# Optimization experiments

Measured on AMD Instinct MI355X. Metric: run time of the kernel, lower is better.

Reference implementation:

```python
import jax, jax.numpy as jnp
import numpy as np

EPS = 1e-6
LN_EPS = 1e-5   # torch nn.LayerNorm default eps
BN_EPS = 1e-5   # torch nn.BatchNorm1d default eps
NUM_HEADS = 8
NEG_SLOPE = 0.0  # leaky=0 in TransformerBlock


def vn_linear(x, W, b, eps=1e-6):
    # x: [B, Cin, 3, N], W: [Cin, Cout], b: [Cout, 3]
    out = jnp.einsum('bidn,io->bodn', x, W)
    u = eps * b / jnp.linalg.norm(b, axis=1, keepdims=True)  # [Cout,3]
    return out + u[None, :, :, None]


def vn_layer_norm(x, gamma, beta):
    # x: [B, C, 3, N]; LayerNorm over channel dim of the vector norms
    norm = jnp.linalg.norm(x, axis=2) + EPS            # [B, C, N]
    t = jnp.swapaxes(norm, 1, 2)                       # [B, N, C]
    mu = t.mean(axis=-1, keepdims=True)
    var = ((t - mu) ** 2).mean(axis=-1, keepdims=True)
    ln = (t - mu) / jnp.sqrt(var + LN_EPS) * gamma + beta
    norm_ln = jnp.swapaxes(ln, 1, 2)                   # [B, C, N]
    return x / norm[:, :, None, :] * norm_ln[:, :, None, :]


def vn_batch_norm(x, gamma, beta):
    # training-mode BatchNorm1d over channel dim of the vector norms
    norm = jnp.linalg.norm(x, axis=2) + EPS            # [B, C, N]
    mu = norm.mean(axis=(0, 2), keepdims=True)         # [1, C, 1]
    var = ((norm - mu) ** 2).mean(axis=(0, 2), keepdims=True)
    bn = (norm - mu) / jnp.sqrt(var + BN_EPS) * gamma[None, :, None] + beta[None, :, None]
    return x / norm[:, :, None, :] * bn[:, :, None, :]


def vn_leaky_relu(x, W, negative_slope=NEG_SLOPE):
    d = jnp.einsum('bidn,io->bodn', x, W)              # learned direction
    dot = (x * d).sum(axis=2, keepdims=True)           # [B, C, 1, N]
    d_norm_sq = (d * d).sum(axis=2, keepdims=True)
    proj = x - dot / (d_norm_sq + EPS) * d
    pos = jnp.where(dot >= 0, x, proj)
    return negative_slope * x + (1.0 - negative_slope) * pos


def attention(Q, K, Z, Wq, bq, Wk, bk, Wz, bz, Wo, bo, num_heads=NUM_HEADS):
    B, C, _, M = Q.shape
    N = K.shape[-1]
    Ch = C // num_heads
    q = vn_linear(Q, Wq, bq).reshape(B, num_heads, Ch, 3, M)
    k = vn_linear(K, Wk, bk).reshape(B, num_heads, Ch, 3, N)
    z = vn_linear(Z, Wz, bz).reshape(B, num_heads, Ch, 3, N)
    # Frobenius inner product: merge (Ch,3) -> F
    qf = q.reshape(B, num_heads, Ch * 3, M)
    kf = k.reshape(B, num_heads, Ch * 3, N)
    const = 1.0 / np.sqrt(3 * Ch)
    scores = const * jnp.einsum('bhfm,bhfn->bhmn', qf, kf)
    A = jax.nn.softmax(scores, axis=-1)
    out = jnp.einsum('bhcdn,bhmn->bhcdm', z, A).reshape(B, C, 3, M)
    return vn_linear(out, Wo, bo)


def forward(x, Wq, bq, Wk, bk, Wz, bz, Wo, bo, ln1_g, ln1_b,
            Wm1, bm1, bn_g, bn_b, Wr, Wm2, bm2, ln2_g, ln2_b):
    queries = x
    y = attention(queries, x, x, Wq, bq, Wk, bk, Wz, bz, Wo, bo)
    y = vn_layer_norm(y, ln1_g, ln1_b)
    y = y + queries
    identity = y
    h = vn_linear(y, Wm1, bm1)
    h = vn_batch_norm(h, bn_g, bn_b)
    h = vn_leaky_relu(h, Wr)
    h = vn_linear(h, Wm2, bm2)
    h = vn_layer_norm(h, ln2_g, ln2_b)
    return h + identity


def setup_inputs() -> dict:
    key = jax.random.key(0)
    ks = list(jax.random.split(key, 16))
    B, C, N = 8, 256, 1024
    bound = 1.0 / np.sqrt(C)

    def lin(k, fin, fout):
        k1, k2 = jax.random.split(k)
        W = jax.random.uniform(k1, (fin, fout), minval=-bound, maxval=bound, dtype=jnp.float32)
        b = jax.random.uniform(k2, (fout, 3), minval=-bound, maxval=bound, dtype=jnp.float32)
        return W, b

    x = jax.random.normal(ks[0], (B, C, 3, N), dtype=jnp.float32)
    Wq, bq = lin(ks[1], C, C)
    Wk, bk = lin(ks[2], C, C)
    Wz, bz = lin(ks[3], C, C)
    Wo, bo = lin(ks[4], C, C)
    Wm1, bm1 = lin(ks[5], C, C)
    Wm2, bm2 = lin(ks[6], C, C)
    Wr = jax.random.uniform(ks[7], (C, C), minval=-bound, maxval=bound, dtype=jnp.float32)
    ones = jnp.ones((C,), jnp.float32)
    zeros = jnp.zeros((C,), jnp.float32)
    return dict(x=x, Wq=Wq, bq=bq, Wk=Wk, bk=bk, Wz=Wz, bz=bz, Wo=Wo, bo=bo,
                ln1_g=ones, ln1_b=zeros, Wm1=Wm1, bm1=bm1, bn_g=ones, bn_b=zeros,
                Wr=Wr, Wm2=Wm2, bm2=bm2, ln2_g=ones, ln2_b=zeros)


def reference(x, Wq, bq, Wk, bk, Wz, bz, Wo, bo, ln1_g, ln1_b,
              Wm1, bm1, bn_g, bn_b, Wr, Wm2, bm2, ln2_g, ln2_b):
    return forward(x, Wq, bq, Wk, bk, Wz, bz, Wo, bo, ln1_g, ln1_b,
                   Wm1, bm1, bn_g, bn_b, Wr, Wm2, bm2, ln2_g, ln2_b)
```

## Files before the change

kernel.cpp:

```cpp
#include <hip/hip_runtime.h>
#include <math.h>

typedef __attribute__((ext_vector_type(8))) short bf16x8;
typedef __attribute__((ext_vector_type(4))) float f32x4;
typedef unsigned short u16;
typedef __attribute__((ext_vector_type(4))) unsigned short u16x4;
typedef __attribute__((ext_vector_type(8))) unsigned short u16x8;

#define VN_EPS 1e-6f
#define LN_EPS 1e-5f
#define BN_EPS 1e-5f
#define ISQ 0.10206207261596575f

__device__ __forceinline__ u16 f2bf(float f) {
    unsigned u = __builtin_bit_cast(unsigned, f);
    return (u16)((u + 0x7FFFu + ((u >> 16) & 1u)) >> 16);
}
__device__ __forceinline__ float bf2f(u16 h) {
    unsigned u = ((unsigned)h) << 16;
    return __builtin_bit_cast(float, u);
}

__global__ __launch_bounds__(256) void k_u(
    const float* __restrict__ b0, const float* __restrict__ b1,
    const float* __restrict__ b2, const float* __restrict__ b3,
    const float* __restrict__ b4, const float* __restrict__ b5,
    float* __restrict__ uall)
{
    const float* bs[6] = {b0, b1, b2, b3, b4, b5};
    const float* bp = bs[blockIdx.x];
    const int co = threadIdx.x;
    const float v0 = bp[co*3+0], v1 = bp[co*3+1], v2 = bp[co*3+2];
    const float inv = rsqrtf(v0*v0 + v1*v1 + v2*v2);
    float* u = uall + blockIdx.x*768 + co*3;
    u[0] = VN_EPS*v0*inv; u[1] = VN_EPS*v1*inv; u[2] = VN_EPS*v2*inv;
}

__global__ __launch_bounds__(256) void k_wtrans(
    const float* __restrict__ w0, const float* __restrict__ w1,
    const float* __restrict__ w2, const float* __restrict__ w3,
    const float* __restrict__ w4, const float* __restrict__ w5,
    const float* __restrict__ w6, u16* __restrict__ wth, u16* __restrict__ wtl)
{
    const int wi = blockIdx.z;
    const float* W = (wi==0)?w0:(wi==1)?w1:(wi==2)?w2:(wi==3)?w3:(wi==4)?w4:(wi==5)?w5:w6;
    u16* WtH = wth + (long)wi*65536;
    u16* WtL = wtl + (long)wi*65536;
    const int i0 = blockIdx.y*64, o0 = blockIdx.x*64;
    __shared__ float st[64][67];
    const int t = threadIdx.x, q = t >> 6, lane = t & 63;
    for (int j = 0; j < 16; ++j) {
        const int i = q*16 + j;
        st[i][lane] = W[(i0 + i)*256 + o0 + lane];
    }
    __syncthreads();
    for (int j = 0; j < 16; ++j) {
        const int o = q*16 + j;
        const float v = st[lane][o];
        const u16 hi = f2bf(v);
        WtH[(o0 + o)*256 + i0 + lane] = hi;
        WtL[(o0 + o)*256 + i0 + lane] = f2bf(v - bf2f(hi));
    }
}

template<int MODE>
__global__ __launch_bounds__(256) void k_cgemm(
    const float* __restrict__ X, const u16* __restrict__ WtH, const u16* __restrict__ WtL,
    const float* __restrict__ U,
    float* __restrict__ OutF, u16* __restrict__ OutH, u16* __restrict__ OutL)
{
    __shared__ u16 sh[32768];
    const int tid = threadIdx.x;
    const int b = blockIdx.z / 3, d = blockIdx.z % 3;
    const int n0 = blockIdx.x * 64;
    const int co0 = blockIdx.y * 64;

    {
        const int tn = (tid & 15) * 4;
        const int ti = (tid >> 4) * 4;
        #pragma unroll
        for (int it = 0; it < 4; ++it) {
            const int i_l = it*64 + ti;
            const long rb = (((long)(b*256 + i_l))*3 + d)*1024 + n0 + tn;
            const float4 r0 = *(const float4*)&X[rb];
            const float4 r1 = *(const float4*)&X[rb + 3072];
            const float4 r2 = *(const float4*)&X[rb + 6144];
            const float4 r3 = *(const float4*)&X[rb + 9216];
            const float vals[4][4] = {
                {r0.x, r1.x, r2.x, r3.x},
                {r0.y, r1.y, r2.y, r3.y},
                {r0.z, r1.z, r2.z, r3.z},
                {r0.w, r1.w, r2.w, r3.w}};
            #pragma unroll
            for (int j = 0; j < 4; ++j) {
                const int n = tn + j;
                u16x4 hv, lv;
                #pragma unroll
                for (int e = 0; e < 4; ++e) {
                    const float v = vals[j][e];
                    const u16 hi = f2bf(v);
                    hv[e] = hi;
                    lv[e] = f2bf(v - bf2f(hi));
                }
                const int slot = i_l >> 3;
                const int idx = n*256 + ((((slot ^ (n & 7)) << 3)) | (i_l & 4));
                *(u16x4*)&sh[idx] = hv;
                *(u16x4*)&sh[16384 + idx] = lv;
            }
        }
    }
    __syncthreads();

    const int w = tid >> 6, l = tid & 63;
    const int lr = l & 15, lg = l >> 4;

    f32x4 zero = {0.f, 0.f, 0.f, 0.f};
    f32x4 acc[4] = {zero, zero, zero, zero};

    const long arow = (long)(co0 + w*16 + lr)*256 + lg*8;
    #pragma unroll
    for (int s = 0; s < 8; ++s) {
        const bf16x8 ah = *(const bf16x8*)(WtH + arow + s*32);
        const bf16x8 al = *(const bf16x8*)(WtL + arow + s*32);
        #pragma unroll
        for (int ni = 0; ni < 4; ++ni) {
            const int row = ni*16 + lr;
            const int slot = s*4 + lg;
            const int idx = row*256 + ((slot ^ (row & 7)) << 3);
            const bf16x8 bh_ = *(const bf16x8*)&sh[idx];
            const bf16x8 bl_ = *(const bf16x8*)&sh[16384 + idx];
            acc[ni] = __builtin_amdgcn_mfma_f32_16x16x32_bf16(ah, bh_, acc[ni], 0, 0, 0);
            acc[ni] = __builtin_amdgcn_mfma_f32_16x16x32_bf16(ah, bl_, acc[ni], 0, 0, 0);
            acc[ni] = __builtin_amdgcn_mfma_f32_16x16x32_bf16(al, bh_, acc[ni], 0, 0, 0);
        }
    }

    if constexpr (MODE == 0) {
        #pragma unroll
        for (int ni = 0; ni < 4; ++ni)
            #pragma unroll
            for (int r = 0; r < 4; ++r) {
                const int co = co0 + w*16 + lg*4 + r;
                const int nn = n0 + ni*16 + lr;
                float v = acc[ni][r];
                if (U) v += U[co*3 + d];
                OutF[(((long)(b*256 + co))*3 + d)*1024 + nn] = v;
            }
    } else if constexpr (MODE == 1) {
        #pragma unroll
        for (int ni = 0; ni < 4; ++ni)
            #pragma unroll
            for (int r = 0; r < 4; ++r) {
                const int co = co0 + w*16 + lg*4 + r;
                const int nn = n0 + ni*16 + lr;
                float v = acc[ni][r] + U[co*3 + d];
                const long idx = (((long)(b*256 + co))*3 + d)*1024 + nn;
                const u16 hi = f2bf(v);
                OutH[idx] = hi;
                OutL[idx] = f2bf(v - bf2f(hi));
            }
    } else {
        __syncthreads();
        u16* olh = sh;
        u16* oll = sh + 8448;
        #pragma unroll
        for (int ni = 0; ni < 4; ++ni)
            #pragma unroll
            for (int r = 0; r < 4; ++r) {
                const int co_l = w*16 + lg*4 + r;
                float v = acc[ni][r] + U[(co0 + co_l)*3 + d];
                const u16 hi = f2bf(v);
                olh[co_l*66 + ni*16 + lr] = hi;
                oll[co_l*66 + ni*16 + lr] = f2bf(v - bf2f(hi));
            }
        __syncthreads();
        const int n_l = tid & 63, grp = tid >> 6;
        const int h = (co0 >> 5) + (grp >> 1);
        const long base = ((long)(b*8 + h)*1024 + n0 + n_l)*96 + d*32 + (grp & 1)*16;
        u16x8 v0h, v1h, v0l, v1l;
        #pragma unroll
        for (int p = 0; p < 8; ++p) {
            v0h[p] = olh[(grp*16 + p)*66 + n_l];
            v1h[p] = olh[(grp*16 + 8 + p)*66 + n_l];
            v0l[p] = oll[(grp*16 + p)*66 + n_l];
            v1l[p] = oll[(grp*16 + 8 + p)*66 + n_l];
        }
        *(u16x8*)&OutH[base]     = v0h;
        *(u16x8*)&OutH[base + 8] = v1h;
        *(u16x8*)&OutL[base]     = v0l;
        *(u16x8*)&OutL[base + 8] = v1l;
    }
}

__global__ __launch_bounds__(256) void k_attn(
    const u16* __restrict__ Qh, const u16* __restrict__ Ql,
    const u16* __restrict__ Kh, const u16* __restrict__ Kl,
    const u16* __restrict__ Zh, const u16* __restrict__ Zl,
    float* __restrict__ Ao)
{
    const int i = blockIdx.x;
    const int xcd = i & 7;
    const int j = i >> 3;
    const int bh = xcd*8 + (j >> 6);
    const int mt = j & 63;
    const int b = bh >> 3, h = bh & 7;
    const int m0 = mt*16;
    const int tid = threadIdx.x;
    const int w = tid >> 6, l = tid & 63, lr = l & 15, lg = l >> 4;

    __shared__ float S[16*1024];
    __shared__ float outl[16*100];
    __shared__ float inv16[16];

    f32x4 zero = {0.f, 0.f, 0.f, 0.f};

    const long qbase = ((long)bh*1024 + m0 + lr)*96 + lg*8;
    bf16x8 qhf[3], qlf[3];
    #pragma unroll
    for (int s = 0; s < 3; ++s) {
        qhf[s] = *(const bf16x8*)(Qh + qbase + s*32);
        qlf[s] = *(const bf16x8*)(Ql + qbase + s*32);
    }
    for (int nf = 0; nf < 16; ++nf) {
        const int n0 = w*256 + nf*16;
        const long kb = ((long)bh*1024 + n0 + lr)*96 + lg*8;
        f32x4 acc = zero;
        #pragma unroll
        for (int s = 0; s < 3; ++s) {
            const bf16x8 khf = *(const bf16x8*)(Kh + kb + s*32);
            const bf16x8 klf = *(const bf16x8*)(Kl + kb + s*32);
            acc = __builtin_amdgcn_mfma_f32_16x16x32_bf16(qhf[s], khf, acc, 0, 0, 0);
            acc = __builtin_amdgcn_mfma_f32_16x16x32_bf16(qhf[s], klf, acc, 0, 0, 0);
            acc = __builtin_amdgcn_mfma_f32_16x16x32_bf16(qlf[s], khf, acc, 0, 0, 0);
        }
        #pragma unroll
        for (int r = 0; r < 4; ++r)
            S[(lg*4 + r)*1024 + n0 + lr] = acc[r] * ISQ;
    }
    __syncthreads();

    {
        const int r = tid >> 4, s = tid & 15;
        float preg[64];
        float mx = -1e30f;
        #pragma unroll
        for (int j2 = 0; j2 < 64; ++j2) {
            preg[j2] = S[r*1024 + j2*16 + s];
            mx = fmaxf(mx, preg[j2]);
        }
        #pragma unroll
        for (int off = 1; off < 16; off <<= 1)
            mx = fmaxf(mx, __shfl_xor(mx, off));
        float sm = 0.f;
        #pragma unroll
        for (int j2 = 0; j2 < 64; ++j2) {
            const float p = __expf(preg[j2] - mx);
            preg[j2] = p;
            sm += p;
        }
        #pragma unroll
        for (int off = 1; off < 16; off <<= 1)
            sm += __shfl_xor(sm, off);
        if (s == 0) inv16[r] = 1.0f / sm;
        __syncthreads();
        char* Sb = (char*)S;
        #pragma unroll
        for (int j2 = 0; j2 < 64; ++j2) {
            const int n = j2*16 + s;
            const u16 hi = f2bf(preg[j2]);
            const u16 lo = f2bf(preg[j2] - bf2f(hi));
            const int byoff = (n*2) ^ ((r & 7) << 4);
            *(u16*)(Sb + r*4096 + byoff)        = hi;
            *(u16*)(Sb + r*4096 + 2048 + byoff) = lo;
        }
    }
    __syncthreads();

    f32x4 acc2[6];
    #pragma unroll
    for (int f = 0; f < 6; ++f) acc2[f] = zero;
    const long zrow = (long)(b*768 + h*96);
    const char* Sb = (const char*)S;
    for (int kb = 0; kb < 8; ++kb) {
        const int n = w*256 + kb*32 + lg*8;
        const int byoff = lr*4096 + (((n*2)) ^ ((lr & 7) << 4));
        const bf16x8 ph = *(const bf16x8*)(Sb + byoff);
        const bf16x8 pl = *(const bf16x8*)(Sb + byoff + 2048);
        #pragma unroll
        for (int ff = 0; ff < 6; ++ff) {
            const long zb = (zrow + ff*16 + lr)*1024 + n;
            const bf16x8 azh = *(const bf16x8*)(Zh + zb);
            const bf16x8 azl = *(const bf16x8*)(Zl + zb);
            acc2[ff] = __builtin_amdgcn_mfma_f32_16x16x32_bf16(ph, azh, acc2[ff], 0, 0, 0);
            acc2[ff] = __builtin_amdgcn_mfma_f32_16x16x32_bf16(ph, azl, acc2[ff], 0, 0, 0);
            acc2[ff] = __builtin_amdgcn_mfma_f32_16x16x32_bf16(pl, azh, acc2[ff], 0, 0, 0);
        }
    }
    __syncthreads();
    for (int wv = 0; wv < 4; ++wv) {
        if (w == wv) {
            #pragma unroll
            for (int ff = 0; ff < 6; ++ff)
                #pragma unroll
                for (int r = 0; r < 4; ++r) {
                    const int m = lg*4 + r, f = ff*16 + lr;
                    if (wv == 0) outl[m*100 + f] = acc2[ff][r];
                    else         outl[m*100 + f] += acc2[ff][r];
                }
        }
        __syncthreads();
    }
    for (int idx = tid; idx < 384; idx += 256) {
        const int f = idx >> 2, mg = idx & 3;
        float4 o;
        o.x = outl[(mg*4+0)*100 + f] * inv16[mg*4+0];
        o.y = outl[(mg*4+1)*100 + f] * inv16[mg*4+1];
        o.z = outl[(mg*4+2)*100 + f] * inv16[mg*4+2];
        o.w = outl[(mg*4+3)*100 + f] * inv16[mg*4+3];
        *(float4*)&Ao[(long)(b*768 + h*96 + f)*1024 + m0 + mg*4] = o;
    }
}

__global__ __launch_bounds__(256) void k_vnln(
    const float* __restrict__ X, const float* __restrict__ Res,
    const float* __restrict__ g, const float* __restrict__ be,
    float* __restrict__ Out)
{
    const int b  = blockIdx.x >> 5;
    const int n  = ((blockIdx.x & 31) << 5) + threadIdx.x;
    const int ty = threadIdx.y;
    const long bbase = (long)b * (256*3*1024);
    float sum = 0.0f, sq = 0.0f;
    for (int ci = 0; ci < 32; ++ci) {
        const int c = (ty << 5) + ci;
        const long base = bbase + (long)c*3072 + n;
        const float x0 = X[base], x1 = X[base+1024], x2 = X[base+2048];
        const float nr = sqrtf(x0*x0 + x1*x1 + x2*x2) + VN_EPS;
        sum += nr; sq += nr*nr;
    }
    __shared__ float s_sum[8][32], s_sq[8][32];
    s_sum[ty][threadIdx.x] = sum; s_sq[ty][threadIdx.x] = sq;
    __syncthreads();
    __shared__ float s_mu[32], s_rs[32];
    if (ty == 0) {
        float S = 0.0f, Q = 0.0f;
        #pragma unroll
        for (int w = 0; w < 8; ++w) { S += s_sum[w][threadIdx.x]; Q += s_sq[w][threadIdx.x]; }
        const float mu = S / 256.0f;
        s_mu[threadIdx.x] = mu;
        s_rs[threadIdx.x] = rsqrtf(Q / 256.0f - mu*mu + LN_EPS);
    }
    __syncthreads();
    const float mu = s_mu[threadIdx.x], rstd = s_rs[threadIdx.x];
    for (int ci = 0; ci < 32; ++ci) {
        const int c = (ty << 5) + ci;
        const long base = bbase + (long)c*3072 + n;
        const float x0 = X[base], x1 = X[base+1024], x2 = X[base+2048];
        const float nr = sqrtf(x0*x0 + x1*x1 + x2*x2) + VN_EPS;
        const float ln = (nr - mu) * rstd * g[c] + be[c];
        const float s  = ln / nr;
        float o0 = x0*s, o1 = x1*s, o2 = x2*s;
        if (Res) { o0 += Res[base]; o1 += Res[base+1024]; o2 += Res[base+2048]; }
        Out[base] = o0; Out[base+1024] = o1; Out[base+2048] = o2;
    }
}

__global__ __launch_bounds__(256) void k_bnstats(
    const float* __restrict__ X, float* __restrict__ bnst)
{
    const int c = blockIdx.x;
    const int t = threadIdx.x;
    float sum = 0.0f, sq = 0.0f;
    for (int b = 0; b < 8; ++b) {
        const long rowbase = ((long)(b*256 + c)) * 3072;
        for (int n0 = 0; n0 < 1024; n0 += 256) {
            const int n = n0 + t;
            const float x0 = X[rowbase + n], x1 = X[rowbase + 1024 + n], x2 = X[rowbase + 2048 + n];
            const float nr = sqrtf(x0*x0 + x1*x1 + x2*x2) + VN_EPS;
            sum += nr; sq += nr*nr;
        }
    }
    #pragma unroll
    for (int off = 32; off > 0; off >>= 1) {
        sum += __shfl_xor(sum, off);
        sq  += __shfl_xor(sq,  off);
    }
    __shared__ float rs[4], rq[4];
    if ((t & 63) == 0) { rs[t >> 6] = sum; rq[t >> 6] = sq; }
    __syncthreads();
    if (t == 0) {
        const float S = rs[0]+rs[1]+rs[2]+rs[3];
        const float Q = rq[0]+rq[1]+rq[2]+rq[3];
        const float mu = S / 8192.0f;
        bnst[c] = mu;
        bnst[256 + c] = rsqrtf(Q / 8192.0f - mu*mu + BN_EPS);
    }
}

__global__ __launch_bounds__(256) void k_bnapply(
    float* __restrict__ X, const float* __restrict__ bnst,
    const float* __restrict__ g, const float* __restrict__ be)
{
    const long i = (long)blockIdx.x * 256 + threadIdx.x;
    const int  n  = (int)(i & 1023);
    const long bc = i >> 10;
    const int  c  = (int)(bc & 255);
    const long base = bc * 3072 + n;
    const float x0 = X[base], x1 = X[base+1024], x2 = X[base+2048];
    const float nr = sqrtf(x0*x0 + x1*x1 + x2*x2) + VN_EPS;
    const float bn = (nr - bnst[c]) * bnst[256 + c] * g[c] + be[c];
    const float s  = bn / nr;
    X[base]      = x0*s;
    X[base+1024] = x1*s;
    X[base+2048] = x2*s;
}

__global__ __launch_bounds__(256) void k_leaky(
    float* __restrict__ X, const float* __restrict__ Dd)
{
    const long i = (long)blockIdx.x * 256 + threadIdx.x;
    const long base = (i >> 10) * 3072 + (i & 1023);
    const float x0 = X[base], x1 = X[base+1024], x2 = X[base+2048];
    const float d0 = Dd[base], d1 = Dd[base+1024], d2 = Dd[base+2048];
    const float dot = x0*d0 + x1*d1 + x2*d2;
    if (dot < 0.0f) {
        const float f = dot / (d0*d0 + d1*d1 + d2*d2 + VN_EPS);
        X[base]      = x0 - f*d0;
        X[base+1024] = x1 - f*d1;
        X[base+2048] = x2 - f*d2;
    }
}

extern "C" void kernel_launch(void* const* d_in, const int* in_sizes, int n_in,
                              void* d_out, int out_size, void* d_ws, size_t ws_size,
                              hipStream_t stream)
{
    const float* x    = (const float*)d_in[0];
    const float* Wq   = (const float*)d_in[1];
    const float* bq   = (const float*)d_in[2];
    const float* Wk   = (const float*)d_in[3];
    const float* bk   = (const float*)d_in[4];
    const float* Wz   = (const float*)d_in[5];
    const float* bz   = (const float*)d_in[6];
    const float* Wo   = (const float*)d_in[7];
    const float* bo   = (const float*)d_in[8];
    const float* ln1g = (const float*)d_in[9];
    const float* ln1b = (const float*)d_in[10];
    const float* Wm1  = (const float*)d_in[11];
    const float* bm1  = (const float*)d_in[12];
    const float* bng  = (const float*)d_in[13];
    const float* bnb  = (const float*)d_in[14];
    const float* Wr   = (const float*)d_in[15];
    const float* Wm2  = (const float*)d_in[16];
    const float* bm2  = (const float*)d_in[17];
    const float* ln2g = (const float*)d_in[18];
    const float* ln2b = (const float*)d_in[19];
    float* out = (float*)d_out;

    char* wsb = (char*)d_ws;
    u16*   qh  = (u16*)(wsb + 0);
    u16*   ql  = (u16*)(wsb + 12582912);
    u16*   kh  = (u16*)(wsb + 25165824);
    u16*   kl  = (u16*)(wsb + 37748736);
    u16*   zh  = (u16*)(wsb + 50331648);
    u16*   zl  = (u16*)(wsb + 62914560);
    u16*   wth = (u16*)(wsb + 109051904);
    u16*   wtl = (u16*)(wsb + 109969408);
    float* uall= (float*)(wsb + 110886912);
    float* bnst= (float*)(wsb + 110905344);
    float* ao  = out;
    float* y0f = (float*)(wsb + 0);
    float* y   = (float*)(wsb + 25165824);
    float* h   = (float*)(wsb + 50331648);
    float* dv  = (float*)(wsb + 75497472);
    float* h2  = (float*)(wsb + 0);

    const dim3 GC(16, 4, 24);

    k_u<<<6, 256, 0, stream>>>(bq, bk, bz, bo, bm1, bm2, uall);
    k_wtrans<<<dim3(4,4,7), 256, 0, stream>>>(Wq, Wk, Wz, Wo, Wm1, Wr, Wm2, wth, wtl);

    k_cgemm<2><<<GC, 256, 0, stream>>>(x, wth + 0*65536, wtl + 0*65536, uall + 0*768, nullptr, qh, ql);
    k_cgemm<2><<<GC, 256, 0, stream>>>(x, wth + 1*65536, wtl + 1*65536, uall + 1*768, nullptr, kh, kl);
    k_cgemm<1><<<GC, 256, 0, stream>>>(x, wth + 2*65536, wtl + 2*65536, uall + 2*768, nullptr, zh, zl);

    k_attn<<<4096, 256, 0, stream>>>(qh, ql, kh, kl, zh, zl, ao);

    k_cgemm<0><<<GC, 256, 0, stream>>>(ao, wth + 3*65536, wtl + 3*65536, uall + 3*768, y0f, nullptr, nullptr);
    k_vnln<<<256, dim3(32,8), 0, stream>>>(y0f, x, ln1g, ln1b, y);

    k_cgemm<0><<<GC, 256, 0, stream>>>(y, wth + 4*65536, wtl + 4*65536, uall + 4*768, h, nullptr, nullptr);
    k_bnstats<<<256, 256, 0, stream>>>(h, bnst);
    k_bnapply<<<8192, 256, 0, stream>>>(h, bnst, bng, bnb);
    k_cgemm<0><<<GC, 256, 0, stream>>>(h, wth + 5*65536, wtl + 5*65536, (const float*)nullptr, dv, nullptr, nullptr);
    k_leaky<<<8192, 256, 0, stream>>>(h, dv);
    k_cgemm<0><<<GC, 256, 0, stream>>>(h, wth + 6*65536, wtl + 6*65536, uall + 5*768, h2, nullptr, nullptr);
    k_vnln<<<256, dim3(32,8), 0, stream>>>(h2, y, ln2g, ln2b, out);
}
```

Baseline: 576.3 us.

## Split attention kernel into two online-softmax chunks to shrink shared memory

The attention kernel now walks the 1024 keys in two chunks of 512 and keeps a running max and sum (online softmax), rescaling the PV accumulators between chunks. This cuts the score buffer from 64KB to 32KB and halves the per-thread probability register array, so more blocks can share a compute unit; launch_bounds is raised to request 4 blocks per CU. It also keeps the three split-precision QK products in separate accumulators. The cost is extra barriers, rescaling work and reloading Q fragments once per chunk.

```diff
diff --git a/kernel.cpp b/kernel.cpp
--- a/kernel.cpp
+++ b/kernel.cpp
@@ -192,7 +192,7 @@
     }
 }
 
-__global__ __launch_bounds__(256) void k_attn(
+__global__ __launch_bounds__(256, 4) void k_attn(
     const u16* __restrict__ Qh, const u16* __restrict__ Ql,
     const u16* __restrict__ Kh, const u16* __restrict__ Kl,
     const u16* __restrict__ Zh, const u16* __restrict__ Zl,
@@ -208,96 +208,116 @@
     const int tid = threadIdx.x;
     const int w = tid >> 6, l = tid & 63, lr = l & 15, lg = l >> 4;
 
-    __shared__ float S[16*1024];
+    __shared__ char Sb[16*2048];
     __shared__ float outl[16*100];
+    __shared__ float fac[16];
     __shared__ float inv16[16];
 
     f32x4 zero = {0.f, 0.f, 0.f, 0.f};
-
-    const long qbase = ((long)bh*1024 + m0 + lr)*96 + lg*8;
-    bf16x8 qhf[3], qlf[3];
-    #pragma unroll
-    for (int s = 0; s < 3; ++s) {
-        qhf[s] = *(const bf16x8*)(Qh + qbase + s*32);
-        qlf[s] = *(const bf16x8*)(Ql + qbase + s*32);
-    }
-    for (int nf = 0; nf < 16; ++nf) {
-        const int n0 = w*256 + nf*16;
-        const long kb = ((long)bh*1024 + n0 + lr)*96 + lg*8;
-        f32x4 acc = zero;
-        #pragma unroll
-        for (int s = 0; s < 3; ++s) {
-            const bf16x8 khf = *(const bf16x8*)(Kh + kb + s*32);
-            const bf16x8 klf = *(const bf16x8*)(Kl + kb + s*32);
-            acc = __builtin_amdgcn_mfma_f32_16x16x32_bf16(qhf[s], khf, acc, 0, 0, 0);
-            acc = __builtin_amdgcn_mfma_f32_16x16x32_bf16(qhf[s], klf, acc, 0, 0, 0);
-            acc = __builtin_amdgcn_mfma_f32_16x16x32_bf16(qlf[s], khf, acc, 0, 0, 0);
-        }
-        #pragma unroll
-        for (int r = 0; r < 4; ++r)
-            S[(lg*4 + r)*1024 + n0 + lr] = acc[r] * ISQ;
-    }
-    __syncthreads();
-
-    {
-        const int r = tid >> 4, s = tid & 15;
-        float preg[64];
-        float mx = -1e30f;
-        #pragma unroll
-        for (int j2 = 0; j2 < 64; ++j2) {
-            preg[j2] = S[r*1024 + j2*16 + s];
-            mx = fmaxf(mx, preg[j2]);
-        }
-        #pragma unroll
-        for (int off = 1; off < 16; off <<= 1)
-            mx = fmaxf(mx, __shfl_xor(mx, off));
-        float sm = 0.f;
-        #pragma unroll
-        for (int j2 = 0; j2 < 64; ++j2) {
-            const float p = __expf(preg[j2] - mx);
-            preg[j2] = p;
-            sm += p;
-        }
-        #pragma unroll
-        for (int off = 1; off < 16; off <<= 1)
-            sm += __shfl_xor(sm, off);
-        if (s == 0) inv16[r] = 1.0f / sm;
-        __syncthreads();
-        char* Sb = (char*)S;
-        #pragma unroll
-        for (int j2 = 0; j2 < 64; ++j2) {
-            const int n = j2*16 + s;
-            const u16 hi = f2bf(preg[j2]);
-            const u16 lo = f2bf(preg[j2] - bf2f(hi));
-            const int byoff = (n*2) ^ ((r & 7) << 4);
-            *(u16*)(Sb + r*4096 + byoff)        = hi;
-            *(u16*)(Sb + r*4096 + 2048 + byoff) = lo;
-        }
-    }
-    __syncthreads();
-
     f32x4 acc2[6];
     #pragma unroll
     for (int f = 0; f < 6; ++f) acc2[f] = zero;
+
+    float run_m = -1e30f, run_l = 0.f;
+    const int r2 = tid >> 4, s2 = tid & 15;
     const long zrow = (long)(b*768 + h*96);
-    const char* Sb = (const char*)S;
-    for (int kb = 0; kb < 8; ++kb) {
-        const int n = w*256 + kb*32 + lg*8;
-        const int byoff = lr*4096 + (((n*2)) ^ ((lr & 7) << 4));
-        const bf16x8 ph = *(const bf16x8*)(Sb + byoff);
-        const bf16x8 pl = *(const bf16x8*)(Sb + byoff + 2048);
-        #pragma unroll
-        for (int ff = 0; ff < 6; ++ff) {
-            const long zb = (zrow + ff*16 + lr)*1024 + n;
-            const bf16x8 azh = *(const bf16x8*)(Zh + zb);
-            const bf16x8 azl = *(const bf16x8*)(Zl + zb);
-            acc2[ff] = __builtin_amdgcn_mfma_f32_16x16x32_bf16(ph, azh, acc2[ff], 0, 0, 0);
-            acc2[ff] = __builtin_amdgcn_mfma_f32_16x16x32_bf16(ph, azl, acc2[ff], 0, 0, 0);
-            acc2[ff] = __builtin_amdgcn_mfma_f32_16x16x32_bf16(pl, azh, acc2[ff], 0, 0, 0);
-        }
-    }
-    __syncthreads();
+    const long qbase = ((long)bh*1024 + m0 + lr)*96 + lg*8;
+
+    for (int c = 0; c < 2; ++c) {
+        __syncthreads();
+
+        {
+            bf16x8 qhf[3], qlf[3];
+            #pragma unroll
+            for (int s = 0; s < 3; ++s) {
+                qhf[s] = *(const bf16x8*)(Qh + qbase + s*32);
+                qlf[s] = *(const bf16x8*)(Ql + qbase + s*32);
+            }
+            for (int nf = 0; nf < 8; ++nf) {
+                const int lcol = w*128 + nf*16;
+                const long kb_ = ((long)bh*1024 + c*512 + lcol + lr)*96 + lg*8;
+                f32x4 aHH = zero, aHL = zero, aLH = zero;
+                #pragma unroll
+                for (int s = 0; s < 3; ++s) {
+                    const bf16x8 khf = *(const bf16x8*)(Kh + kb_ + s*32);
+                    const bf16x8 klf = *(const bf16x8*)(Kl + kb_ + s*32);
+                    aHH = __builtin_amdgcn_mfma_f32_16x16x32_bf16(qhf[s], khf, aHH, 0, 0, 0);
+                    aHL = __builtin_amdgcn_mfma_f32_16x16x32_bf16(qhf[s], klf, aHL, 0, 0, 0);
+                    aLH = __builtin_amdgcn_mfma_f32_16x16x32_bf16(qlf[s], khf, aLH, 0, 0, 0);
+                }
+                #pragma unroll
+                for (int r = 0; r < 4; ++r) {
+                    const int m = lg*4 + r;
+                    const int col = lcol + lr;
+                    const float val = (aHH[r] + aHL[r] + aLH[r]) * ISQ;
+                    *(float*)(Sb + m*2048 + ((col*4) ^ ((m & 7) << 4))) = val;
+                }
+            }
+        }
+        __syncthreads();
+
+        {
+            float v[32];
+            float mx = run_m;
+            #pragma unroll
+            for (int j2 = 0; j2 < 32; ++j2) {
+                const int col = j2*16 + s2;
+                v[j2] = *(const float*)(Sb + r2*2048 + ((col*4) ^ ((r2 & 7) << 4)));
+                mx = fmaxf(mx, v[j2]);
+            }
+            #pragma unroll
+            for (int off = 1; off < 16; off <<= 1)
+                mx = fmaxf(mx, __shfl_xor(mx, off));
+            const float fr = __expf(run_m - mx);
+            float sm = 0.f;
+            #pragma unroll
+            for (int j2 = 0; j2 < 32; ++j2) {
+                const float p = __expf(v[j2] - mx);
+                sm += p;
+                const int col = j2*16 + s2;
+                const int byoff = (col*2) ^ ((r2 & 7) << 4);
+                const u16 hi = f2bf(p);
+                *(u16*)(Sb + r2*2048 + byoff)        = hi;
+                *(u16*)(Sb + r2*2048 + 1024 + byoff) = f2bf(p - bf2f(hi));
+            }
+            #pragma unroll
+            for (int off = 1; off < 16; off <<= 1)
+                sm += __shfl_xor(sm, off);
+            run_l = run_l * fr + sm;
+            run_m = mx;
+            if (s2 == 0) fac[r2] = fr;
+        }
+        __syncthreads();
+
+        #pragma unroll
+        for (int r = 0; r < 4; ++r) {
+            const float fm = fac[lg*4 + r];
+            #pragma unroll
+            for (int ff = 0; ff < 6; ++ff) acc2[ff][r] *= fm;
+        }
+
+        for (int kb = 0; kb < 4; ++kb) {
+            const int lcol = w*128 + kb*32 + lg*8;
+            const int byoff = lr*2048 + ((lcol*2) ^ ((lr & 7) << 4));
+            const bf16x8 ph = *(const bf16x8*)(Sb + byoff);
+            const bf16x8 pl = *(const bf16x8*)(Sb + byoff + 1024);
+            const long gn = c*512 + lcol;
+            #pragma unroll
+            for (int ff = 0; ff < 6; ++ff) {
+                const long zb = (zrow + ff*16 + lr)*1024 + gn;
+                const bf16x8 azh = *(const bf16x8*)(Zh + zb);
+                const bf16x8 azl = *(const bf16x8*)(Zl + zb);
+                acc2[ff] = __builtin_amdgcn_mfma_f32_16x16x32_bf16(ph, azh, acc2[ff], 0, 0, 0);
+                acc2[ff] = __builtin_amdgcn_mfma_f32_16x16x32_bf16(ph, azl, acc2[ff], 0, 0, 0);
+                acc2[ff] = __builtin_amdgcn_mfma_f32_16x16x32_bf16(pl, azh, acc2[ff], 0, 0, 0);
+            }
+        }
+    }
+
+    if (s2 == 0) inv16[r2] = 1.0f / run_l;
+
     for (int wv = 0; wv < 4; ++wv) {
+        __syncthreads();
         if (w == wv) {
             #pragma unroll
             for (int ff = 0; ff < 6; ++ff)
@@ -308,8 +328,8 @@
                     else         outl[m*100 + f] += acc2[ff][r];
                 }
         }
-        __syncthreads();
-    }
+    }
+    __syncthreads();
     for (int idx = tid; idx < 384; idx += 256) {
         const int f = idx >> 2, mg = idx & 3;
         float4 o;
```

Measured after the change: 829.6 us. +44.0%, slower.

## Replace materialized-score attention with flash-style online softmax per wave

Applied to the files above, without the earlier changes.

The attention kernel no longer writes the full 16x1024 score tile to shared memory, reduces it, and splits the N range across waves. Each wave now owns 16 query rows and streams all 64 key tiles with a running max and sum. It uses the MFMA output (transposed score) directly as the A operand of a 16x16x16 MFMA against Z, so shared memory and block syncs disappear and fewer blocks are launched. The cost is per-tile rescaling, exp and shuffle overhead, and more Z global reads, since each wave re-reads Z for its own rows.

```diff
diff --git a/kernel.cpp b/kernel.cpp
--- a/kernel.cpp
+++ b/kernel.cpp
@@ -2,6 +2,7 @@
 #include <math.h>
 
 typedef __attribute__((ext_vector_type(8))) short bf16x8;
+typedef __attribute__((ext_vector_type(4))) short bf16x4;
 typedef __attribute__((ext_vector_type(4))) float f32x4;
 typedef unsigned short u16;
 typedef __attribute__((ext_vector_type(4))) unsigned short u16x4;
@@ -201,18 +202,17 @@
     const int i = blockIdx.x;
     const int xcd = i & 7;
     const int j = i >> 3;
-    const int bh = xcd*8 + (j >> 6);
-    const int mt = j & 63;
+    const int bh = xcd*8 + (j >> 4);
+    const int mt = j & 15;
     const int b = bh >> 3, h = bh & 7;
-    const int m0 = mt*16;
     const int tid = threadIdx.x;
     const int w = tid >> 6, l = tid & 63, lr = l & 15, lg = l >> 4;
-
-    __shared__ float S[16*1024];
-    __shared__ float outl[16*100];
-    __shared__ float inv16[16];
+    const int m0 = mt*64 + w*16;
 
     f32x4 zero = {0.f, 0.f, 0.f, 0.f};
+    f32x4 acc2[6];
+    #pragma unroll
+    for (int f = 0; f < 6; ++f) acc2[f] = zero;
 
     const long qbase = ((long)bh*1024 + m0 + lr)*96 + lg*8;
     bf16x8 qhf[3], qlf[3];
@@ -221,103 +221,78 @@
         qhf[s] = *(const bf16x8*)(Qh + qbase + s*32);
         qlf[s] = *(const bf16x8*)(Ql + qbase + s*32);
     }
-    for (int nf = 0; nf < 16; ++nf) {
-        const int n0 = w*256 + nf*16;
-        const long kb = ((long)bh*1024 + n0 + lr)*96 + lg*8;
-        f32x4 acc = zero;
+
+    const long zrow = (long)(b*768 + h*96);
+    float run_m = -1e30f, run_l = 0.f;
+
+    for (int t = 0; t < 64; ++t) {
+        const long kb = ((long)bh*1024 + t*16 + lr)*96 + lg*8;
+        f32x4 sacc = zero;
         #pragma unroll
         for (int s = 0; s < 3; ++s) {
             const bf16x8 khf = *(const bf16x8*)(Kh + kb + s*32);
             const bf16x8 klf = *(const bf16x8*)(Kl + kb + s*32);
-            acc = __builtin_amdgcn_mfma_f32_16x16x32_bf16(qhf[s], khf, acc, 0, 0, 0);
-            acc = __builtin_amdgcn_mfma_f32_16x16x32_bf16(qhf[s], klf, acc, 0, 0, 0);
-            acc = __builtin_amdgcn_mfma_f32_16x16x32_bf16(qlf[s], khf, acc, 0, 0, 0);
-        }
-        #pragma unroll
-        for (int r = 0; r < 4; ++r)
-            S[(lg*4 + r)*1024 + n0 + lr] = acc[r] * ISQ;
-    }
-    __syncthreads();
-
-    {
-        const int r = tid >> 4, s = tid & 15;
-        float preg[64];
-        float mx = -1e30f;
-        #pragma unroll
-        for (int j2 = 0; j2 < 64; ++j2) {
-            preg[j2] = S[r*1024 + j2*16 + s];
-            mx = fmaxf(mx, preg[j2]);
-        }
-        #pragma unroll
-        for (int off = 1; off < 16; off <<= 1)
-            mx = fmaxf(mx, __shfl_xor(mx, off));
-        float sm = 0.f;
-        #pragma unroll
-        for (int j2 = 0; j2 < 64; ++j2) {
-            const float p = __expf(preg[j2] - mx);
-            preg[j2] = p;
-            sm += p;
-        }
-        #pragma unroll
-        for (int off = 1; off < 16; off <<= 1)
-            sm += __shfl_xor(sm, off);
-        if (s == 0) inv16[r] = 1.0f / sm;
-        __syncthreads();
-        char* Sb = (char*)S;
-        #pragma unroll
-        for (int j2 = 0; j2 < 64; ++j2) {
-            const int n = j2*16 + s;
-            const u16 hi = f2bf(preg[j2]);
-            const u16 lo = f2bf(preg[j2] - bf2f(hi));
-            const int byoff = (n*2) ^ ((r & 7) << 4);
-            *(u16*)(Sb + r*4096 + byoff)        = hi;
-            *(u16*)(Sb + r*4096 + 2048 + byoff) = lo;
-        }
-    }
-    __syncthreads();
-
-    f32x4 acc2[6];
-    #pragma unroll
-    for (int f = 0; f < 6; ++f) acc2[f] = zero;
-    const long zrow = (long)(b*768 + h*96);
-    const char* Sb = (const char*)S;
-    for (int kb = 0; kb < 8; ++kb) {
-        const int n = w*256 + kb*32 + lg*8;
-        const int byoff = lr*4096 + (((n*2)) ^ ((lr & 7) << 4));
-        const bf16x8 ph = *(const bf16x8*)(Sb + byoff);
-        const bf16x8 pl = *(const bf16x8*)(Sb + byoff + 2048);
+            sacc = __builtin_amdgcn_mfma_f32_16x16x32_bf16(khf, qhf[s], sacc, 0, 0, 0);
+            sacc = __builtin_amdgcn_mfma_f32_16x16x32_bf16(khf, qlf[s], sacc, 0, 0, 0);
+            sacc = __builtin_amdgcn_mfma_f32_16x16x32_bf16(klf, qhf[s], sacc, 0, 0, 0);
+        }
+        const float s0 = sacc[0]*ISQ, s1 = sacc[1]*ISQ, s2 = sacc[2]*ISQ, s3 = sacc[3]*ISQ;
+
+        float tmax = fmaxf(fmaxf(s0, s1), fmaxf(s2, s3));
+        tmax = fmaxf(tmax, __shfl_xor(tmax, 16));
+        tmax = fmaxf(tmax, __shfl_xor(tmax, 32));
+        const float m_new = fmaxf(run_m, tmax);
+        const float fr = __expf(run_m - m_new);
+        const float p0 = __expf(s0 - m_new);
+        const float p1 = __expf(s1 - m_new);
+        const float p2 = __expf(s2 - m_new);
+        const float p3 = __expf(s3 - m_new);
+        float tsum = (p0 + p1) + (p2 + p3);
+        tsum += __shfl_xor(tsum, 16);
+        tsum += __shfl_xor(tsum, 32);
+        run_l = run_l * fr + tsum;
+        run_m = m_new;
+
+        #pragma unroll
+        for (int r = 0; r < 4; ++r) {
+            const float fm = __shfl(fr, lg*4 + r);
+            #pragma unroll
+            for (int ff = 0; ff < 6; ++ff) acc2[ff][r] *= fm;
+        }
+
+        bf16x4 phv, plv;
+        {
+            const u16 h0 = f2bf(p0), h1 = f2bf(p1), h2 = f2bf(p2), h3 = f2bf(p3);
+            phv[0] = (short)h0; phv[1] = (short)h1; phv[2] = (short)h2; phv[3] = (short)h3;
+            plv[0] = (short)f2bf(p0 - bf2f(h0));
+            plv[1] = (short)f2bf(p1 - bf2f(h1));
+            plv[2] = (short)f2bf(p2 - bf2f(h2));
+            plv[3] = (short)f2bf(p3 - bf2f(h3));
+        }
+
         #pragma unroll
         for (int ff = 0; ff < 6; ++ff) {
-            const long zb = (zrow + ff*16 + lr)*1024 + n;
-            const bf16x8 azh = *(const bf16x8*)(Zh + zb);
-            const bf16x8 azl = *(const bf16x8*)(Zl + zb);
-            acc2[ff] = __builtin_amdgcn_mfma_f32_16x16x32_bf16(ph, azh, acc2[ff], 0, 0, 0);
-            acc2[ff] = __builtin_amdgcn_mfma_f32_16x16x32_bf16(ph, azl, acc2[ff], 0, 0, 0);
-            acc2[ff] = __builtin_amdgcn_mfma_f32_16x16x32_bf16(pl, azh, acc2[ff], 0, 0, 0);
-        }
-    }
-    __syncthreads();
-    for (int wv = 0; wv < 4; ++wv) {
-        if (w == wv) {
-            #pragma unroll
-            for (int ff = 0; ff < 6; ++ff)
-                #pragma unroll
-                for (int r = 0; r < 4; ++r) {
-                    const int m = lg*4 + r, f = ff*16 + lr;
-                    if (wv == 0) outl[m*100 + f] = acc2[ff][r];
-                    else         outl[m*100 + f] += acc2[ff][r];
-                }
-        }
-        __syncthreads();
-    }
-    for (int idx = tid; idx < 384; idx += 256) {
-        const int f = idx >> 2, mg = idx & 3;
+            const long zb = (zrow + ff*16 + lr)*1024 + t*16 + lg*4;
+            const bf16x4 zh4 = *(const bf16x4*)(Zh + zb);
+            const bf16x4 zl4 = *(const bf16x4*)(Zl + zb);
+            acc2[ff] = __builtin_amdgcn_mfma_f32_16x16x16bf16_1k(phv, zh4, acc2[ff], 0, 0, 0);
+            acc2[ff] = __builtin_amdgcn_mfma_f32_16x16x16bf16_1k(phv, zl4, acc2[ff], 0, 0, 0);
+            acc2[ff] = __builtin_amdgcn_mfma_f32_16x16x16bf16_1k(plv, zh4, acc2[ff], 0, 0, 0);
+        }
+    }
+
+    const float lrec = 1.0f / run_l;
+    #pragma unroll
+    for (int r = 0; r < 4; ++r) {
+        const float iv = __shfl(lrec, lg*4 + r);
+        #pragma unroll
+        for (int ff = 0; ff < 6; ++ff) acc2[ff][r] *= iv;
+    }
+    #pragma unroll
+    for (int ff = 0; ff < 6; ++ff) {
         float4 o;
-        o.x = outl[(mg*4+0)*100 + f] * inv16[mg*4+0];
-        o.y = outl[(mg*4+1)*100 + f] * inv16[mg*4+1];
-        o.z = outl[(mg*4+2)*100 + f] * inv16[mg*4+2];
-        o.w = outl[(mg*4+3)*100 + f] * inv16[mg*4+3];
-        *(float4*)&Ao[(long)(b*768 + h*96 + f)*1024 + m0 + mg*4] = o;
+        o.x = acc2[ff][0]; o.y = acc2[ff][1]; o.z = acc2[ff][2]; o.w = acc2[ff][3];
+        *(float4*)&Ao[(zrow + ff*16 + lr)*1024 + m0 + lg*4] = o;
     }
 }
 
@@ -484,7 +459,7 @@
     k_cgemm<2><<<GC, 256, 0, stream>>>(x, wth + 1*65536, wtl + 1*65536, uall + 1*768, nullptr, kh, kl);
     k_cgemm<1><<<GC, 256, 0, stream>>>(x, wth + 2*65536, wtl + 2*65536, uall + 2*768, nullptr, zh, zl);
 
-    k_attn<<<4096, 256, 0, stream>>>(qh, ql, kh, kl, zh, zl, ao);
+    k_attn<<<1024, 256, 0, stream>>>(qh, ql, kh, kl, zh, zl, ao);
 
     k_cgemm<0><<<GC, 256, 0, stream>>>(ao, wth + 3*65536, wtl + 3*65536, uall + 3*768, y0f, nullptr, nullptr);
     k_vnln<<<256, dim3(32,8), 0, stream>>>(y0f, x, ln1g, ln1b, y);
```

Result: slower. 839.7 us (+45.7%).

## Keep attention scores in registers and drop shared-memory score matrix

Applied to the files above, without the earlier changes.

Computes the transposed score tiles (K·Q) so each lane holds scores for one query row, then does the softmax max and sum in registers with small cross-wave reductions instead of staging a 16x1024 float score matrix in shared memory. The bf16 hi/lo probability fragments stay in registers and feed 16x16x16 MFMAs directly, which removes the large LDS buffer, its swizzled stores and loads, and a barrier. The cost is much higher register pressure from the 16 score tiles plus the probability fragments, which may reduce occupancy or cause spills. The PV step also switches to narrower K=16 MFMAs with 4-element Z loads, so it issues more, smaller loads.

```diff
diff --git a/kernel.cpp b/kernel.cpp
--- a/kernel.cpp
+++ b/kernel.cpp
@@ -2,6 +2,7 @@
 #include <math.h>
 
 typedef __attribute__((ext_vector_type(8))) short bf16x8;
+typedef __attribute__((ext_vector_type(4))) short bf16x4;
 typedef __attribute__((ext_vector_type(4))) float f32x4;
 typedef unsigned short u16;
 typedef __attribute__((ext_vector_type(4))) unsigned short u16x4;
@@ -208,9 +209,10 @@
     const int tid = threadIdx.x;
     const int w = tid >> 6, l = tid & 63, lr = l & 15, lg = l >> 4;
 
-    __shared__ float S[16*1024];
+    __shared__ float smx[4][16];
+    __shared__ float ssum[4][16];
+    __shared__ float inv16[16];
     __shared__ float outl[16*100];
-    __shared__ float inv16[16];
 
     f32x4 zero = {0.f, 0.f, 0.f, 0.f};
 
@@ -221,82 +223,74 @@
         qhf[s] = *(const bf16x8*)(Qh + qbase + s*32);
         qlf[s] = *(const bf16x8*)(Ql + qbase + s*32);
     }
-    for (int nf = 0; nf < 16; ++nf) {
-        const int n0 = w*256 + nf*16;
-        const long kb = ((long)bh*1024 + n0 + lr)*96 + lg*8;
-        f32x4 acc = zero;
+
+    f32x4 sc[16];
+    const long kbase = ((long)bh*1024 + w*256 + lr)*96 + lg*8;
+    #pragma unroll
+    for (int t = 0; t < 16; ++t) {
+        const long kb = kbase + (long)t*16*96;
+        f32x4 a = zero;
         #pragma unroll
         for (int s = 0; s < 3; ++s) {
             const bf16x8 khf = *(const bf16x8*)(Kh + kb + s*32);
             const bf16x8 klf = *(const bf16x8*)(Kl + kb + s*32);
-            acc = __builtin_amdgcn_mfma_f32_16x16x32_bf16(qhf[s], khf, acc, 0, 0, 0);
-            acc = __builtin_amdgcn_mfma_f32_16x16x32_bf16(qhf[s], klf, acc, 0, 0, 0);
-            acc = __builtin_amdgcn_mfma_f32_16x16x32_bf16(qlf[s], khf, acc, 0, 0, 0);
-        }
+            a = __builtin_amdgcn_mfma_f32_16x16x32_bf16(khf, qhf[s], a, 0, 0, 0);
+            a = __builtin_amdgcn_mfma_f32_16x16x32_bf16(khf, qlf[s], a, 0, 0, 0);
+            a = __builtin_amdgcn_mfma_f32_16x16x32_bf16(klf, qhf[s], a, 0, 0, 0);
+        }
+        sc[t] = a;
+    }
+
+    float mx = -1e30f;
+    #pragma unroll
+    for (int t = 0; t < 16; ++t)
         #pragma unroll
         for (int r = 0; r < 4; ++r)
-            S[(lg*4 + r)*1024 + n0 + lr] = acc[r] * ISQ;
-    }
-    __syncthreads();
-
-    {
-        const int r = tid >> 4, s = tid & 15;
-        float preg[64];
-        float mx = -1e30f;
-        #pragma unroll
-        for (int j2 = 0; j2 < 64; ++j2) {
-            preg[j2] = S[r*1024 + j2*16 + s];
-            mx = fmaxf(mx, preg[j2]);
-        }
-        #pragma unroll
-        for (int off = 1; off < 16; off <<= 1)
-            mx = fmaxf(mx, __shfl_xor(mx, off));
-        float sm = 0.f;
-        #pragma unroll
-        for (int j2 = 0; j2 < 64; ++j2) {
-            const float p = __expf(preg[j2] - mx);
-            preg[j2] = p;
+            mx = fmaxf(mx, sc[t][r]);
+    mx = fmaxf(mx, __shfl_xor(mx, 16));
+    mx = fmaxf(mx, __shfl_xor(mx, 32));
+    if (lg == 0) smx[w][lr] = mx;
+    __syncthreads();
+    mx = fmaxf(fmaxf(smx[0][lr], smx[1][lr]), fmaxf(smx[2][lr], smx[3][lr]));
+
+    bf16x4 phv[16], plv[16];
+    float sm = 0.f;
+    #pragma unroll
+    for (int t = 0; t < 16; ++t) {
+        #pragma unroll
+        for (int r = 0; r < 4; ++r) {
+            const float p = __expf((sc[t][r] - mx) * ISQ);
             sm += p;
-        }
-        #pragma unroll
-        for (int off = 1; off < 16; off <<= 1)
-            sm += __shfl_xor(sm, off);
-        if (s == 0) inv16[r] = 1.0f / sm;
-        __syncthreads();
-        char* Sb = (char*)S;
-        #pragma unroll
-        for (int j2 = 0; j2 < 64; ++j2) {
-            const int n = j2*16 + s;
-            const u16 hi = f2bf(preg[j2]);
-            const u16 lo = f2bf(preg[j2] - bf2f(hi));
-            const int byoff = (n*2) ^ ((r & 7) << 4);
-            *(u16*)(Sb + r*4096 + byoff)        = hi;
-            *(u16*)(Sb + r*4096 + 2048 + byoff) = lo;
-        }
-    }
-    __syncthreads();
+            const u16 hi = f2bf(p);
+            phv[t][r] = (short)hi;
+            plv[t][r] = (short)f2bf(p - bf2f(hi));
+        }
+    }
+    sm += __shfl_xor(sm, 16);
+    sm += __shfl_xor(sm, 32);
+    if (lg == 0) ssum[w][lr] = sm;
+    __syncthreads();
+    if (w == 0 && lg == 0)
+        inv16[lr] = 1.0f / (ssum[0][lr] + ssum[1][lr] + ssum[2][lr] + ssum[3][lr]);
 
     f32x4 acc2[6];
     #pragma unroll
     for (int f = 0; f < 6; ++f) acc2[f] = zero;
     const long zrow = (long)(b*768 + h*96);
-    const char* Sb = (const char*)S;
-    for (int kb = 0; kb < 8; ++kb) {
-        const int n = w*256 + kb*32 + lg*8;
-        const int byoff = lr*4096 + (((n*2)) ^ ((lr & 7) << 4));
-        const bf16x8 ph = *(const bf16x8*)(Sb + byoff);
-        const bf16x8 pl = *(const bf16x8*)(Sb + byoff + 2048);
+    #pragma unroll
+    for (int t = 0; t < 16; ++t) {
+        const int n = w*256 + t*16 + lg*4;
         #pragma unroll
         for (int ff = 0; ff < 6; ++ff) {
             const long zb = (zrow + ff*16 + lr)*1024 + n;
-            const bf16x8 azh = *(const bf16x8*)(Zh + zb);
-            const bf16x8 azl = *(const bf16x8*)(Zl + zb);
-            acc2[ff] = __builtin_amdgcn_mfma_f32_16x16x32_bf16(ph, azh, acc2[ff], 0, 0, 0);
-            acc2[ff] = __builtin_amdgcn_mfma_f32_16x16x32_bf16(ph, azl, acc2[ff], 0, 0, 0);
-            acc2[ff] = __builtin_amdgcn_mfma_f32_16x16x32_bf16(pl, azh, acc2[ff], 0, 0, 0);
-        }
-    }
-    __syncthreads();
+            const bf16x4 zh4 = *(const bf16x4*)(Zh + zb);
+            const bf16x4 zl4 = *(const bf16x4*)(Zl + zb);
+            acc2[ff] = __builtin_amdgcn_mfma_f32_16x16x16bf16_1k(phv[t], zh4, acc2[ff], 0, 0, 0);
+            acc2[ff] = __builtin_amdgcn_mfma_f32_16x16x16bf16_1k(phv[t], zl4, acc2[ff], 0, 0, 0);
+            acc2[ff] = __builtin_amdgcn_mfma_f32_16x16x16bf16_1k(plv[t], zh4, acc2[ff], 0, 0, 0);
+        }
+    }
+
     for (int wv = 0; wv < 4; ++wv) {
         if (w == wv) {
             #pragma unroll
```

Measured after the change: 767.5 us. 1.33x slower.
